# Optimization experiments

Measured on AMD Instinct MI355X. Metric: run time of the kernel, lower is better.

Reference implementation:

```python
import jax, jax.numpy as jnp
import numpy as np

B, Q, HID = 8, 8, 4096
H, KVH, D = 32, 8, 128
KV = 4096
ROPE_THETA = 10000.0


def rotate_half(x):
    x1, x2 = jnp.split(x, 2, axis=-1)
    return jnp.concatenate([-x2, x1], axis=-1)


def setup_inputs() -> dict:
    key = jax.random.key(0)
    ks = jax.random.split(key, 6)
    hidden_states = jax.random.normal(ks[0], (B, Q, HID), dtype=jnp.float32)
    position_ids = jnp.broadcast_to(jnp.arange(KV, dtype=jnp.int64), (B, KV))
    key_cache = jax.random.normal(ks[1], (B, KVH, KV, D), dtype=jnp.float32)
    value_cache = jax.random.normal(ks[2], (B, KVH, KV, D), dtype=jnp.float32)
    # mask: True -> blocked (-10000). Queries occupy last Q positions, causal.
    qpos = KV - Q + jnp.arange(Q)
    attention_mask = (jnp.arange(KV)[None, :] > qpos[:, None])[None, None]  # [1,1,Q,KV]
    attention_mask = jnp.broadcast_to(attention_mask, (B, 1, Q, KV))
    q_w = jax.random.normal(ks[3], (HID, HID), dtype=jnp.float32) * 0.02
    o_w = jax.random.normal(ks[4], (HID, HID), dtype=jnp.float32) * 0.02
    return {"hidden_states": hidden_states, "position_ids": position_ids,
            "key_cache": key_cache, "value_cache": value_cache,
            "attention_mask": attention_mask, "q_w": q_w, "o_w": o_w}


def reference(hidden_states, position_ids, key_cache, value_cache, attention_mask, q_w, o_w):
    # q projection: nn.Linear -> x @ W^T
    q = hidden_states @ q_w.T                       # [B,Q,HID]
    q = q.reshape(B, Q, H, D).transpose(0, 2, 1, 3)  # [B,H,Q,D]

    # rotary tables for kv_seq_len positions
    half = D // 2
    inv_freq = 1.0 / (ROPE_THETA ** (jnp.arange(0, half, dtype=jnp.float32) / half))
    t = jnp.arange(KV, dtype=jnp.float32)
    freqs = t[:, None] * inv_freq[None, :]           # [KV, D/2]
    emb = jnp.concatenate([freqs, freqs], axis=-1)   # [KV, D]
    cos_t, sin_t = jnp.cos(emb), jnp.sin(emb)

    # position_idx trick from the module: single effective rope position
    idx = jnp.argmax(position_ids.astype(jnp.int32), axis=1)[0]
    pid = jnp.take(position_ids, idx[None], axis=1)  # [B,1]
    cos = cos_t[pid][:, None]                        # [B,1,1,D]
    sin = sin_t[pid][:, None]
    q = q * cos + rotate_half(q) * sin               # [B,H,Q,D]

    # GQA attention without materializing repeat_kv (same math)
    G = H // KVH
    qg = q.reshape(B, KVH, G, Q, D)
    scores = jnp.einsum('bkgqd,bksd->bkgqs', qg, key_cache) / jnp.sqrt(jnp.float32(D))
    mask = attention_mask[:, :, None]                # [B,1,1,Q,KV]
    scores = jnp.where(mask, jnp.float32(-10000.0), scores)
    probs = jax.nn.softmax(scores.astype(jnp.float32), axis=-1).astype(q.dtype)
    out = jnp.einsum('bkgqs,bksd->bkgqd', probs, value_cache)  # [B,KVH,G,Q,D]
    out = out.reshape(B, H, Q, D).transpose(0, 2, 1, 3).reshape(B, Q, HID)
    return out @ o_w.T
```

## Files before the change

### kernel.cpp

```cpp
#include <hip/hip_runtime.h>
#include <math.h>

#define B_   8
#define Q_   8
#define HID  4096
#define NH   32
#define KVH_ 8
#define GQ   4
#define D_   128
#define KV_  4096
#define M_   64

#define OFF_COS   0
#define OFF_SIN   512
#define OFF_QROPE 1024
#define OFF_ATT   (OFF_QROPE + M_*HID)
#define OFF_OPART (OFF_ATT + M_*HID)
#define OFF_MPART (OFF_OPART + 64*8*32*128)
#define OFF_LPART (OFF_MPART + 64*8*32)
#define OFF_GPART (OFF_LPART + 64*8*32)

typedef __attribute__((ext_vector_type(8))) short short8;
typedef __attribute__((ext_vector_type(4))) float f32x4;

__global__ void prep_kernel(const int* __restrict__ pos, float* __restrict__ ws) {
    __shared__ int sv[256], si[256];
    __shared__ int s_idx;
    int t = threadIdx.x;
    int bv = -2147483647 - 1, bi = 0x7fffffff;
    for (int i = t; i < KV_; i += 256) {
        int v = pos[i];
        if (v > bv || (v == bv && i < bi)) { bv = v; bi = i; }
    }
    sv[t] = bv; si[t] = bi;
    __syncthreads();
    for (int off = 128; off > 0; off >>= 1) {
        if (t < off) {
            int v2 = sv[t + off], i2 = si[t + off];
            if (v2 > sv[t] || (v2 == sv[t] && i2 < si[t])) { sv[t] = v2; si[t] = i2; }
        }
        __syncthreads();
    }
    if (t == 0) s_idx = si[0];
    __syncthreads();
    int idx = s_idx;
    for (int u = t; u < B_ * 64; u += 256) {
        int b = u >> 6, d = u & 63;
        int pid = pos[b * KV_ + idx];
        float inv = __expf(-(float)d * (9.210340371976184f / 64.0f));
        float f = (float)pid * inv;
        ws[OFF_COS + u] = cosf(f);
        ws[OFF_SIN + u] = sinf(f);
    }
}

__device__ __forceinline__ unsigned f2bf_rne(float x) {
    unsigned u = __float_as_uint(x);
    return (u + 0x7fffu + ((u >> 16) & 1u)) >> 16;
}
__device__ __forceinline__ float bf2f(unsigned h) { return __uint_as_float(h << 16); }

__device__ __forceinline__ void cvt_store(unsigned short* __restrict__ ph,
                                          unsigned short* __restrict__ pl,
                                          int r, int q, const float4* v) {
    unsigned hi[16], lo[16];
    const float* f = (const float*)v;
    #pragma unroll
    for (int i = 0; i < 16; ++i) {
        float x = f[i];
        unsigned h = f2bf_rne(x);
        hi[i] = h;
        lo[i] = f2bf_rne(x - bf2f(h));
    }
    int s = r & 7;
    #pragma unroll
    for (int hf = 0; hf < 2; ++hf) {
        int o = 2 * q + hf;
        const unsigned* H = hi + hf * 8;
        const unsigned* L = lo + hf * 8;
        uint4 hv, lv;
        hv.x = H[0] | (H[1] << 16); hv.y = H[2] | (H[3] << 16);
        hv.z = H[4] | (H[5] << 16); hv.w = H[6] | (H[7] << 16);
        lv.x = L[0] | (L[1] << 16); lv.y = L[2] | (L[3] << 16);
        lv.z = L[4] | (L[5] << 16); lv.w = L[6] | (L[7] << 16);
        *(uint4*)(ph + (size_t)r * 64 + ((o ^ s) * 8)) = hv;
        *(uint4*)(pl + (size_t)r * 64 + ((o ^ s) * 8)) = lv;
    }
}

__global__ __launch_bounds__(256) void gemm_part(const float* __restrict__ A,
                                                 const float* __restrict__ W,
                                                 float* __restrict__ part) {
    __shared__ __align__(16) unsigned short AH[2][64][64];
    __shared__ __align__(16) unsigned short AL[2][64][64];
    __shared__ __align__(16) unsigned short WH[2][64][64];
    __shared__ __align__(16) unsigned short WL[2][64][64];

    int nc = blockIdx.x, kc = blockIdx.y;
    int t = threadIdx.x;
    int k0 = kc * 256, n0 = nc * 64;
    int sr = t & 63, sq = t >> 6;
    const float* arow = A + (size_t)sr * HID + k0 + sq * 16;
    const float* wrow = W + (size_t)(n0 + sr) * HID + k0 + sq * 16;

    f32x4 acc[4];
    #pragma unroll
    for (int ct = 0; ct < 4; ++ct) acc[ct] = (f32x4){0.f, 0.f, 0.f, 0.f};

    {
        float4 va[4], vw[4];
        #pragma unroll
        for (int c = 0; c < 4; ++c) {
            va[c] = *(const float4*)(arow + c * 4);
            vw[c] = *(const float4*)(wrow + c * 4);
        }
        cvt_store(&AH[0][0][0], &AL[0][0][0], sr, sq, va);
        cvt_store(&WH[0][0][0], &WL[0][0][0], sr, sq, vw);
    }
    __syncthreads();

    int w = t >> 6, l = t & 63;
    int rA = 16 * w + (l & 15);
    int sA = rA & 7;
    int lq = l >> 4;
    int cur = 0;

    for (int kt = 0; kt < 4; ++kt) {
        float4 va[4], vw[4];
        if (kt < 3) {
            #pragma unroll
            for (int c = 0; c < 4; ++c) {
                va[c] = *(const float4*)(arow + (kt + 1) * 64 + c * 4);
                vw[c] = *(const float4*)(wrow + (kt + 1) * 64 + c * 4);
            }
        }
        #pragma unroll
        for (int ks = 0; ks < 2; ++ks) {
            int oct = ks * 4 + lq;
            short8 ah = *(const short8*)&AH[cur][rA][(oct ^ sA) * 8];
            short8 al = *(const short8*)&AL[cur][rA][(oct ^ sA) * 8];
            #pragma unroll
            for (int ct = 0; ct < 4; ++ct) {
                int nB = ct * 16 + (l & 15);
                int sB = nB & 7;
                short8 bh = *(const short8*)&WH[cur][nB][(oct ^ sB) * 8];
                short8 bl = *(const short8*)&WL[cur][nB][(oct ^ sB) * 8];
                acc[ct] = __builtin_amdgcn_mfma_f32_16x16x32_bf16(ah, bh, acc[ct], 0, 0, 0);
                acc[ct] = __builtin_amdgcn_mfma_f32_16x16x32_bf16(ah, bl, acc[ct], 0, 0, 0);
                acc[ct] = __builtin_amdgcn_mfma_f32_16x16x32_bf16(al, bh, acc[ct], 0, 0, 0);
            }
        }
        if (kt < 3) {
            int nb = cur ^ 1;
            cvt_store(&AH[nb][0][0], &AL[nb][0][0], sr, sq, va);
            cvt_store(&WH[nb][0][0], &WL[nb][0][0], sr, sq, vw);
            __syncthreads();
            cur = nb;
        }
    }

    #pragma unroll
    for (int ct = 0; ct < 4; ++ct) {
        int n = n0 + ct * 16 + (l & 15);
        #pragma unroll
        for (int i = 0; i < 4; ++i) {
            int m = 16 * w + lq * 4 + i;
            part[((size_t)kc * 64 + m) * HID + n] = acc[ct][i];
        }
    }
}

__global__ void qrope_kernel(float* ws) {
    const float* part = ws + OFF_GPART;
    int blk = blockIdx.x;
    int b = blk >> 5, h = blk & 31;
    int t = threadIdx.x;
    int qq = t >> 5, dl = t & 31;
    int m = b * 8 + qq;
    int d0 = dl * 2;
    float x0 = 0, x1 = 0, y0 = 0, y1 = 0;
    const float* pbase = part + (size_t)m * HID + h * 128;
    #pragma unroll
    for (int kc = 0; kc < 16; ++kc) {
        const float* p = pbase + (size_t)kc * 64 * HID;
        x0 += p[d0];      x1 += p[d0 + 1];
        y0 += p[d0 + 64]; y1 += p[d0 + 65];
    }
    float c0 = ws[OFF_COS + b * 64 + d0], c1 = ws[OFF_COS + b * 64 + d0 + 1];
    float s0 = ws[OFF_SIN + b * 64 + d0], s1 = ws[OFF_SIN + b * 64 + d0 + 1];
    float* qr = ws + OFF_QROPE + ((size_t)(b * 32 + h)) * Q_ * D_ + (size_t)qq * D_;
    qr[d0]      = x0 * c0 - y0 * s0;
    qr[d0 + 1]  = x1 * c1 - y1 * s1;
    qr[d0 + 64] = y0 * c0 + x0 * s0;
    qr[d0 + 65] = y1 * c1 + x1 * s1;
}

#define CHUNK 512
#define TK 64
__global__ __launch_bounds__(256) void attn_kernel(const float* __restrict__ Kc,
                                                   const float* __restrict__ Vc,
                                                   float* __restrict__ ws) {
    __shared__ __align__(16) float qT[128][36];
    __shared__ __align__(16) float kT[128][68];
    __shared__ __align__(16) float pT[64][36];
    __shared__ float m_st[32], l_st[32], al_st[32];

    int c = blockIdx.x, kvh = blockIdx.y, b = blockIdx.z;
    int t = threadIdx.x;
    int pair = b * 8 + kvh;
    const float* qbase = ws + OFF_QROPE + (size_t)pair * 32 * 128;
    {
        int r = t & 31, qh = t >> 5;
        #pragma unroll
        for (int cq = 0; cq < 4; ++cq) {
            int dq = qh + cq * 8;
            float4 v = *(const float4*)(qbase + (size_t)r * 128 + dq * 4);
            qT[dq*4+0][r] = v.x; qT[dq*4+1][r] = v.y;
            qT[dq*4+2][r] = v.z; qT[dq*4+3][r] = v.w;
        }
    }
    if (t < 32) { m_st[t] = -INFINITY; l_st[t] = 0.f; }

    int st = t & 15;
    int dh = (t >> 4) & 1;
    int rt = t >> 5;
    int dt = t & 31;

    float o[4][4];
    #pragma unroll
    for (int i = 0; i < 4; i++)
        #pragma unroll
        for (int j = 0; j < 4; j++) o[i][j] = 0.f;

    const float* Kb = Kc + ((size_t)pair * KV_ + c * CHUNK) * D_;
    const float* Vb = Vc + ((size_t)pair * KV_ + c * CHUNK) * D_;
    const float scale = 0.08838834764831845f;

    for (int T = 0; T < CHUNK / TK; ++T) {
        int s0 = T * TK;
        __syncthreads();
        {
            int s = t >> 2, qr = t & 3;
            const float* kr = Kb + (size_t)(s0 + s) * D_ + qr * 4;
            #pragma unroll
            for (int cq = 0; cq < 8; ++cq) {
                float4 v = *(const float4*)(kr + cq * 16);
                int d = qr * 4 + cq * 16;
                kT[d+0][s] = v.x; kT[d+1][s] = v.y;
                kT[d+2][s] = v.z; kT[d+3][s] = v.w;
            }
        }
        __syncthreads();
        float S[4][4];
        #pragma unroll
        for (int i = 0; i < 4; i++)
            #pragma unroll
            for (int j = 0; j < 4; j++) S[i][j] = 0.f;
        int dbase = dh * 64;
        #pragma unroll 4
        for (int dd = 0; dd < 64; ++dd) {
            int d = dbase + dd;
            float4 q4 = *(const float4*)&qT[d][rt * 4];
            float4 k4 = *(const float4*)&kT[d][st * 4];
            float qa[4] = {q4.x, q4.y, q4.z, q4.w};
            float ka[4] = {k4.x, k4.y, k4.z, k4.w};
            #pragma unroll
            for (int i = 0; i < 4; i++)
            #pragma unroll
            for (int j = 0; j < 4; j++)
                S[i][j] += qa[i] * ka[j];
        }
        #pragma unroll
        for (int i = 0; i < 4; i++)
            #pragma unroll
            for (int j = 0; j < 4; j++)
                S[i][j] += __shfl_xor(S[i][j], 16, 64);
        int sabs_base = c * CHUNK + s0 + st * 4;
        #pragma unroll
        for (int i = 0; i < 4; i++) {
            int r = rt * 4 + i;
            int qq = r & 7;
            int qpos = KV_ - Q_ + qq;
            float v[4];
            float rmax = -INFINITY;
            #pragma unroll
            for (int j = 0; j < 4; j++) {
                int sa = sabs_base + j;
                float x = (sa > qpos) ? -10000.0f : S[i][j] * scale;
                v[j] = x;
                rmax = fmaxf(rmax, x);
            }
            for (int ml = 1; ml <= 8; ml <<= 1) rmax = fmaxf(rmax, __shfl_xor(rmax, ml, 64));
            float m_old = m_st[r];
            float m_new = fmaxf(m_old, rmax);
            float al = __expf(m_old - m_new);
            float ps = 0.f;
            #pragma unroll
            for (int j = 0; j < 4; j++) {
                float p = __expf(v[j] - m_new);
                if (dh == 0) pT[st * 4 + j][r] = p;
                ps += p;
            }
            for (int ml = 1; ml <= 8; ml <<= 1) ps += __shfl_xor(ps, ml, 64);
            if (st == 0 && dh == 0) {
                l_st[r] = l_st[r] * al + ps;
                m_st[r] = m_new;
                al_st[r] = al;
            }
        }
        __syncthreads();
        float al4[4];
        #pragma unroll
        for (int i = 0; i < 4; i++) al4[i] = al_st[rt * 4 + i];
        #pragma unroll
        for (int i = 0; i < 4; i++)
            #pragma unroll
            for (int j = 0; j < 4; j++) o[i][j] *= al4[i];
        const float* Vg = Vb + (size_t)s0 * D_ + dt * 4;
        #pragma unroll 8
        for (int s = 0; s < TK; ++s) {
            float4 p4 = *(const float4*)&pT[s][rt * 4];
            float4 v4 = *(const float4*)(Vg + (size_t)s * D_);
            float pp[4] = {p4.x, p4.y, p4.z, p4.w};
            float vv[4] = {v4.x, v4.y, v4.z, v4.w};
            #pragma unroll
            for (int i = 0; i < 4; i++)
            #pragma unroll
            for (int j = 0; j < 4; j++)
                o[i][j] += pp[i] * vv[j];
        }
    }
    float* opart = ws + OFF_OPART + ((size_t)pair * 8 + c) * 32 * 128;
    #pragma unroll
    for (int i = 0; i < 4; i++) {
        int r = rt * 4 + i;
        float* dst = opart + (size_t)r * 128 + dt * 4;
        float4 v;
        v.x = o[i][0]; v.y = o[i][1]; v.z = o[i][2]; v.w = o[i][3];
        *(float4*)dst = v;
    }
    __syncthreads();
    if (t < 32) {
        ws[OFF_MPART + ((size_t)pair * 8 + c) * 32 + t] = m_st[t];
        ws[OFF_LPART + ((size_t)pair * 8 + c) * 32 + t] = l_st[t];
    }
}

__global__ void combine_kernel(float* ws) {
    __shared__ float w_sh[8][32];
    int pair = blockIdx.x;
    int b = pair >> 3, kvh = pair & 7;
    int t = threadIdx.x;
    if (t < 32) {
        int r = t;
        float M = -INFINITY;
        float mv[8];
        #pragma unroll
        for (int cc = 0; cc < 8; ++cc) {
            mv[cc] = ws[OFF_MPART + ((size_t)pair * 8 + cc) * 32 + r];
            M = fmaxf(M, mv[cc]);
        }
        float L = 0.f;
        float e[8];
        #pragma unroll
        for (int cc = 0; cc < 8; ++cc) {
            e[cc] = __expf(mv[cc] - M);
            L += e[cc] * ws[OFF_LPART + ((size_t)pair * 8 + cc) * 32 + r];
        }
        float invL = 1.f / L;
        #pragma unroll
        for (int cc = 0; cc < 8; ++cc) w_sh[cc][r] = e[cc] * invL;
    }
    __syncthreads();
    const float* opart = ws + OFF_OPART + (size_t)pair * 8 * 32 * 128;
    float* aout = ws + OFF_ATT;
    for (int idx = t; idx < 32 * 128; idx += 256) {
        int r = idx >> 7, d = idx & 127;
        float acc = 0.f;
        #pragma unroll
        for (int cc = 0; cc < 8; ++cc)
            acc += w_sh[cc][r] * opart[((size_t)cc * 32 + r) * 128 + d];
        int g = r >> 3, qq = r & 7;
        aout[((size_t)(b * 8 + qq)) * HID + (kvh * 4 + g) * 128 + d] = acc;
    }
}

__global__ void oreduce_kernel(const float* __restrict__ part, float* __restrict__ out) {
    int idx = blockIdx.x * 256 + threadIdx.x;
    float4 acc = {0, 0, 0, 0};
    const float4* p = (const float4*)part;
    #pragma unroll
    for (int kc = 0; kc < 16; ++kc) {
        float4 v = p[(size_t)kc * 65536 + idx];
        acc.x += v.x; acc.y += v.y; acc.z += v.z; acc.w += v.w;
    }
    ((float4*)out)[idx] = acc;
}

extern "C" void kernel_launch(void* const* d_in, const int* in_sizes, int n_in,
                              void* d_out, int out_size, void* d_ws, size_t ws_size,
                              hipStream_t stream) {
    const float* hidden = (const float*)d_in[0];
    const int*   pos    = (const int*)d_in[1];
    const float* kcache = (const float*)d_in[2];
    const float* vcache = (const float*)d_in[3];
    const float* qw = (const float*)d_in[5];
    const float* ow = (const float*)d_in[6];
    float* ws  = (float*)d_ws;
    float* out = (float*)d_out;
    float* gpart = ws + OFF_GPART;

    prep_kernel<<<1, 256, 0, stream>>>(pos, ws);
    gemm_part<<<dim3(64, 16), 256, 0, stream>>>(hidden, qw, gpart);
    qrope_kernel<<<256, 256, 0, stream>>>(ws);
    attn_kernel<<<dim3(8, 8, 8), 256, 0, stream>>>(kcache, vcache, ws);
    combine_kernel<<<64, 256, 0, stream>>>(ws);
    gemm_part<<<dim3(64, 16), 256, 0, stream>>>(ws + OFF_ATT, ow, gpart);
    oreduce_kernel<<<256, 256, 0, stream>>>(gpart, out);
}
```

Before: 461.2 us.

## Coalesce GEMM tile loads, halve split-K, and prefetch K tiles in attention

The GEMM staging loads change so that 16 consecutive threads read one contiguous 64-float row segment, giving coalesced global reads instead of per-thread 64-byte strided chunks. The split-K factor drops from 16 to 8, so each block walks 512 K-elements and fewer partial sums are written and then reduced. The attention kernel now register-prefetches the next K tile while the current one is stored to shared memory, overlapping global latency with compute. Fewer split-K blocks (512 instead of 1024) lowers the GEMM's parallelism across CUs, and the prefetch adds register pressure.

```diff
diff --git a/kernel.cpp b/kernel.cpp
--- a/kernel.cpp
+++ b/kernel.cpp
@@ -10,6 +10,8 @@
 #define D_   128
 #define KV_  4096
 #define M_   64
+
+#define KC_  8
 
 #define OFF_COS   0
 #define OFF_SIN   512
@@ -60,32 +62,16 @@
 }
 __device__ __forceinline__ float bf2f(unsigned h) { return __uint_as_float(h << 16); }
 
-__device__ __forceinline__ void cvt_store(unsigned short* __restrict__ ph,
-                                          unsigned short* __restrict__ pl,
-                                          int r, int q, const float4* v) {
-    unsigned hi[16], lo[16];
-    const float* f = (const float*)v;
-    #pragma unroll
-    for (int i = 0; i < 16; ++i) {
-        float x = f[i];
-        unsigned h = f2bf_rne(x);
-        hi[i] = h;
-        lo[i] = f2bf_rne(x - bf2f(h));
-    }
-    int s = r & 7;
-    #pragma unroll
-    for (int hf = 0; hf < 2; ++hf) {
-        int o = 2 * q + hf;
-        const unsigned* H = hi + hf * 8;
-        const unsigned* L = lo + hf * 8;
-        uint4 hv, lv;
-        hv.x = H[0] | (H[1] << 16); hv.y = H[2] | (H[3] << 16);
-        hv.z = H[4] | (H[5] << 16); hv.w = H[6] | (H[7] << 16);
-        lv.x = L[0] | (L[1] << 16); lv.y = L[2] | (L[3] << 16);
-        lv.z = L[4] | (L[5] << 16); lv.w = L[6] | (L[7] << 16);
-        *(uint4*)(ph + (size_t)r * 64 + ((o ^ s) * 8)) = hv;
-        *(uint4*)(pl + (size_t)r * 64 + ((o ^ s) * 8)) = lv;
-    }
+__device__ __forceinline__ void cvt4(float4 v, uint2* h2, uint2* l2) {
+    float f[4] = {v.x, v.y, v.z, v.w};
+    unsigned h[4], l[4];
+    #pragma unroll
+    for (int i = 0; i < 4; ++i) {
+        h[i] = f2bf_rne(f[i]);
+        l[i] = f2bf_rne(f[i] - bf2f(h[i]));
+    }
+    h2->x = h[0] | (h[1] << 16); h2->y = h[2] | (h[3] << 16);
+    l2->x = l[0] | (l[1] << 16); l2->y = l[2] | (l[3] << 16);
 }
 
 __global__ __launch_bounds__(256) void gemm_part(const float* __restrict__ A,
@@ -98,24 +84,29 @@
 
     int nc = blockIdx.x, kc = blockIdx.y;
     int t = threadIdx.x;
-    int k0 = kc * 256, n0 = nc * 64;
-    int sr = t & 63, sq = t >> 6;
-    const float* arow = A + (size_t)sr * HID + k0 + sq * 16;
-    const float* wrow = W + (size_t)(n0 + sr) * HID + k0 + sq * 16;
+    int k0 = kc * 512, n0 = nc * 64;
+    int f4 = t & 15;
+    int rb = t >> 4;
+    int oct = f4 >> 1;
+    int sub = (f4 & 1) * 4;
 
     f32x4 acc[4];
     #pragma unroll
     for (int ct = 0; ct < 4; ++ct) acc[ct] = (f32x4){0.f, 0.f, 0.f, 0.f};
 
     {
-        float4 va[4], vw[4];
-        #pragma unroll
-        for (int c = 0; c < 4; ++c) {
-            va[c] = *(const float4*)(arow + c * 4);
-            vw[c] = *(const float4*)(wrow + c * 4);
-        }
-        cvt_store(&AH[0][0][0], &AL[0][0][0], sr, sq, va);
-        cvt_store(&WH[0][0][0], &WL[0][0][0], sr, sq, vw);
+        #pragma unroll
+        for (int i = 0; i < 4; ++i) {
+            int r = rb + 16 * i;
+            float4 va = *(const float4*)(A + (size_t)r * HID + k0 + f4 * 4);
+            float4 vw = *(const float4*)(W + (size_t)(n0 + r) * HID + k0 + f4 * 4);
+            int slot = ((oct ^ (r & 7)) * 8 + sub);
+            uint2 h2, l2;
+            cvt4(va, &h2, &l2);
+            *(uint2*)&AH[0][r][slot] = h2; *(uint2*)&AL[0][r][slot] = l2;
+            cvt4(vw, &h2, &l2);
+            *(uint2*)&WH[0][r][slot] = h2; *(uint2*)&WL[0][r][slot] = l2;
+        }
     }
     __syncthreads();
 
@@ -125,35 +116,44 @@
     int lq = l >> 4;
     int cur = 0;
 
-    for (int kt = 0; kt < 4; ++kt) {
+    for (int kt = 0; kt < 8; ++kt) {
         float4 va[4], vw[4];
-        if (kt < 3) {
-            #pragma unroll
-            for (int c = 0; c < 4; ++c) {
-                va[c] = *(const float4*)(arow + (kt + 1) * 64 + c * 4);
-                vw[c] = *(const float4*)(wrow + (kt + 1) * 64 + c * 4);
+        if (kt < 7) {
+            #pragma unroll
+            for (int i = 0; i < 4; ++i) {
+                int r = rb + 16 * i;
+                va[i] = *(const float4*)(A + (size_t)r * HID + k0 + (kt + 1) * 64 + f4 * 4);
+                vw[i] = *(const float4*)(W + (size_t)(n0 + r) * HID + k0 + (kt + 1) * 64 + f4 * 4);
             }
         }
         #pragma unroll
         for (int ks = 0; ks < 2; ++ks) {
-            int oct = ks * 4 + lq;
-            short8 ah = *(const short8*)&AH[cur][rA][(oct ^ sA) * 8];
-            short8 al = *(const short8*)&AL[cur][rA][(oct ^ sA) * 8];
+            int o2 = ks * 4 + lq;
+            short8 ah = *(const short8*)&AH[cur][rA][(o2 ^ sA) * 8];
+            short8 al = *(const short8*)&AL[cur][rA][(o2 ^ sA) * 8];
             #pragma unroll
             for (int ct = 0; ct < 4; ++ct) {
                 int nB = ct * 16 + (l & 15);
                 int sB = nB & 7;
-                short8 bh = *(const short8*)&WH[cur][nB][(oct ^ sB) * 8];
-                short8 bl = *(const short8*)&WL[cur][nB][(oct ^ sB) * 8];
+                short8 bh = *(const short8*)&WH[cur][nB][(o2 ^ sB) * 8];
+                short8 bl = *(const short8*)&WL[cur][nB][(o2 ^ sB) * 8];
                 acc[ct] = __builtin_amdgcn_mfma_f32_16x16x32_bf16(ah, bh, acc[ct], 0, 0, 0);
                 acc[ct] = __builtin_amdgcn_mfma_f32_16x16x32_bf16(ah, bl, acc[ct], 0, 0, 0);
                 acc[ct] = __builtin_amdgcn_mfma_f32_16x16x32_bf16(al, bh, acc[ct], 0, 0, 0);
             }
         }
-        if (kt < 3) {
+        if (kt < 7) {
             int nb = cur ^ 1;
-            cvt_store(&AH[nb][0][0], &AL[nb][0][0], sr, sq, va);
-            cvt_store(&WH[nb][0][0], &WL[nb][0][0], sr, sq, vw);
+            #pragma unroll
+            for (int i = 0; i < 4; ++i) {
+                int r = rb + 16 * i;
+                int slot = ((oct ^ (r & 7)) * 8 + sub);
+                uint2 h2, l2;
+                cvt4(va[i], &h2, &l2);
+                *(uint2*)&AH[nb][r][slot] = h2; *(uint2*)&AL[nb][r][slot] = l2;
+                cvt4(vw[i], &h2, &l2);
+                *(uint2*)&WH[nb][r][slot] = h2; *(uint2*)&WL[nb][r][slot] = l2;
+            }
             __syncthreads();
             cur = nb;
         }
@@ -181,7 +181,7 @@
     float x0 = 0, x1 = 0, y0 = 0, y1 = 0;
     const float* pbase = part + (size_t)m * HID + h * 128;
     #pragma unroll
-    for (int kc = 0; kc < 16; ++kc) {
+    for (int kc = 0; kc < KC_; ++kc) {
         const float* p = pbase + (size_t)kc * 64 * HID;
         x0 += p[d0];      x1 += p[d0 + 1];
         y0 += p[d0 + 64]; y1 += p[d0 + 65];
@@ -236,19 +236,29 @@
     const float* Vb = Vc + ((size_t)pair * KV_ + c * CHUNK) * D_;
     const float scale = 0.08838834764831845f;
 
+    int sk = t >> 2, qr = t & 3;
+    float4 kreg[8];
+    {
+        const float* kr = Kb + (size_t)sk * D_ + qr * 4;
+        #pragma unroll
+        for (int cq = 0; cq < 8; ++cq) kreg[cq] = *(const float4*)(kr + cq * 16);
+    }
+
     for (int T = 0; T < CHUNK / TK; ++T) {
         int s0 = T * TK;
         __syncthreads();
         {
-            int s = t >> 2, qr = t & 3;
-            const float* kr = Kb + (size_t)(s0 + s) * D_ + qr * 4;
             #pragma unroll
             for (int cq = 0; cq < 8; ++cq) {
-                float4 v = *(const float4*)(kr + cq * 16);
                 int d = qr * 4 + cq * 16;
-                kT[d+0][s] = v.x; kT[d+1][s] = v.y;
-                kT[d+2][s] = v.z; kT[d+3][s] = v.w;
-            }
+                kT[d+0][sk] = kreg[cq].x; kT[d+1][sk] = kreg[cq].y;
+                kT[d+2][sk] = kreg[cq].z; kT[d+3][sk] = kreg[cq].w;
+            }
+        }
+        if (T < CHUNK / TK - 1) {
+            const float* kr = Kb + (size_t)((T + 1) * TK + sk) * D_ + qr * 4;
+            #pragma unroll
+            for (int cq = 0; cq < 8; ++cq) kreg[cq] = *(const float4*)(kr + cq * 16);
         }
         __syncthreads();
         float S[4][4];
@@ -390,7 +400,7 @@
     float4 acc = {0, 0, 0, 0};
     const float4* p = (const float4*)part;
     #pragma unroll
-    for (int kc = 0; kc < 16; ++kc) {
+    for (int kc = 0; kc < KC_; ++kc) {
         float4 v = p[(size_t)kc * 65536 + idx];
         acc.x += v.x; acc.y += v.y; acc.z += v.z; acc.w += v.w;
     }
@@ -411,10 +421,10 @@
     float* gpart = ws + OFF_GPART;
 
     prep_kernel<<<1, 256, 0, stream>>>(pos, ws);
-    gemm_part<<<dim3(64, 16), 256, 0, stream>>>(hidden, qw, gpart);
+    gemm_part<<<dim3(64, KC_), 256, 0, stream>>>(hidden, qw, gpart);
     qrope_kernel<<<256, 256, 0, stream>>>(ws);
     attn_kernel<<<dim3(8, 8, 8), 256, 0, stream>>>(kcache, vcache, ws);
     combine_kernel<<<64, 256, 0, stream>>>(ws);
-    gemm_part<<<dim3(64, 16), 256, 0, stream>>>(ws + OFF_ATT, ow, gpart);
+    gemm_part<<<dim3(64, KC_), 256, 0, stream>>>(ws + OFF_ATT, ow, gpart);
     oreduce_kernel<<<256, 256, 0, stream>>>(gpart, out);
 }
```

Measured after the change: 432.8 us. -6.2%, faster.
